# Optimization experiments

Measured on AMD Instinct MI355X. Metric: run time of the kernel, lower is better.

## Reference

```python
import jax, jax.numpy as jnp
import numpy as np

SCALING = 32.0 / 16.0  # alpha / rank


def _nf4_levels():
    # q_i = Phi^{-1}((i+0.5)/16), normalized to [-1, 1]
    i = jnp.arange(16, dtype=jnp.float32)
    p = jnp.clip((i + 0.5) / 16.0, 1e-6, 1.0 - 1e-6)
    lv = jnp.sqrt(2.0) * jax.scipy.special.erfinv(2.0 * p - 1.0)
    return lv / jnp.max(jnp.abs(lv))


def _dequantize(q_weight, scales):
    # q_weight: (out, in//2) packed nibbles; scales: (out, num_groups)
    out_f, packed = q_weight.shape
    in_f = packed * 2
    hi = (q_weight >> 4) & 15
    lo = q_weight & 15
    idx = jnp.stack([hi, lo], axis=-1).reshape(out_f, in_f)  # interleave hi/lo
    w = _nf4_levels()[idx]  # (out, in)
    num_groups = scales.shape[1]
    block = in_f // num_groups
    w = (w.reshape(out_f, num_groups, block) * scales[:, :, None].astype(jnp.float32))
    return w.reshape(out_f, in_f)


def setup_inputs() -> dict:
    key = jax.random.key(0)
    k1, k2, k3, k4, k5 = jax.random.split(key, 5)
    B, S, IN, OUT, R, BLK = 4, 64, 8192, 8192, 16, 64
    x = jax.random.normal(k1, (B, S, IN), dtype=jnp.float32)
    q_weight = jax.random.randint(k2, (OUT, IN // 2), 0, 256, dtype=jnp.int32)
    scales = jax.random.uniform(k3, (OUT, IN // BLK), dtype=jnp.float32) * 0.02 + 1e-4
    lora_A = jax.random.normal(k4, (R, IN), dtype=jnp.float32) * 0.02
    lora_B = jax.random.normal(k5, (OUT, R), dtype=jnp.float32) * 0.02
    return {"x": x, "q_weight": q_weight, "scales": scales,
            "lora_A": lora_A, "lora_B": lora_B}


def reference(x, q_weight, scales, lora_A, lora_B):
    w = _dequantize(q_weight, scales)               # (out, in) fp32
    base = jnp.einsum('bsi,oi->bso', x, w)          # F.linear(x, W)
    lora = jnp.einsum('bsi,ri->bsr', x, lora_A)     # x @ A^T (dropout p=0)
    lora = jnp.einsum('bsr,or->bso', lora, lora_B)  # @ B^T
    return base + SCALING * lora
```

## Files before the change

### kernel.cpp

```cpp
#include <hip/hip_runtime.h>
#include <hip/hip_bf16.h>
#include <stdint.h>

typedef __attribute__((ext_vector_type(4))) float f32x4;
typedef __attribute__((ext_vector_type(8))) short short8;
typedef __attribute__((ext_vector_type(4))) int int4v;

#define IN_F   8192
#define OUT_F  8192
#define MROWS  256
#define BN     64
#define BK     64
#define NGRP   128
#define KTILES 32

__device__ unsigned short g_xb[MROWS * IN_F];
__device__ float          g_t[MROWS * 16];
__device__ float          g_part[4 * MROWS * OUT_F];

__device__ __constant__ float NF4_LVL[16] = {
  -1.0f,        -0.70756721f, -0.54221982f, -0.41681853f,
  -0.31090474f, -0.21594601f, -0.12734085f, -0.04209530f,
   0.04209530f,  0.12734085f,  0.21594601f,  0.31090474f,
   0.41681853f,  0.54221982f,  0.70756721f,  1.0f };

static __device__ inline uint32_t pkbf(float a, float b) {
  __bf16 ha = (__bf16)a, hb = (__bf16)b;
  return (uint32_t)__builtin_bit_cast(unsigned short, ha)
       | ((uint32_t)__builtin_bit_cast(unsigned short, hb) << 16);
}

__global__ __launch_bounds__(256) void k_convert(const float* __restrict__ x) {
  int d = blockIdx.x * 256 + threadIdx.x;
  int l15 = d & 15, sub = (d >> 4) & 3, kk = (d >> 6) & 1;
  int m16 = (d >> 7) & 15, kt = d >> 11;
  int r = m16 * 16 + l15;
  int k = kt * 64 + (kk * 4 + sub) * 8;
  const float* src = x + (size_t)r * IN_F + k;
  f32x4 v0 = *(const f32x4*)src;
  f32x4 v1 = *(const f32x4*)(src + 4);
  int4v ov;
  ov[0] = (int)pkbf(v0.x, v0.y); ov[1] = (int)pkbf(v0.z, v0.w);
  ov[2] = (int)pkbf(v1.x, v1.y); ov[3] = (int)pkbf(v1.z, v1.w);
  *(int4v*)(g_xb + (size_t)d * 8) = ov;
}

__global__ __launch_bounds__(256) void k_xa(const float* __restrict__ x,
                                            const float* __restrict__ lora_A) {
  int m = blockIdx.x, tid = threadIdx.x;
  float acc[16];
#pragma unroll
  for (int r = 0; r < 16; ++r) acc[r] = 0.f;
  const float* xr = x + (size_t)m * IN_F;
  for (int it = 0; it < 8; ++it) {
    int k = (tid + it * 256) * 4;
    f32x4 xv = *(const f32x4*)(xr + k);
#pragma unroll
    for (int r = 0; r < 16; ++r) {
      f32x4 av = *(const f32x4*)(lora_A + (size_t)r * IN_F + k);
      acc[r] += xv.x * av.x + xv.y * av.y + xv.z * av.z + xv.w * av.w;
    }
  }
#pragma unroll
  for (int r = 0; r < 16; ++r) {
    float v = acc[r];
#pragma unroll
    for (int off = 32; off; off >>= 1) v += __shfl_xor(v, off, 64);
    acc[r] = v;
  }
  __shared__ float sm[4][16];
  int lane = tid & 63, wave = tid >> 6;
  if (lane == 0) {
#pragma unroll
    for (int r = 0; r < 16; ++r) sm[wave][r] = acc[r];
  }
  __syncthreads();
  if (tid < 16)
    g_t[m * 16 + tid] = 2.0f * (sm[0][tid] + sm[1][tid] + sm[2][tid] + sm[3][tid]);
}

__global__ __launch_bounds__(512, 4) void k_gemm(
    const int* __restrict__ qw, const float* __restrict__ scales)
{
  __shared__ unsigned short Bl[2][BN * BK];
  __shared__ float lut16[16];

  int tid = threadIdx.x;
  int lane = tid & 63, wave = tid >> 6;
  if (tid < 16) lut16[tid] = NF4_LVL[tid];

  int flat = blockIdx.x;
  int wg = (flat & 7) * 64 + (flat >> 3);
  int bx = wg & 127, bz = wg >> 7;
  int n0 = bx * BN;
  int ktg0 = bz * KTILES;

  int dn = tid >> 3, dc = tid & 7;
  const int* qr = qw + (size_t)(n0 + dn) * (IN_F / 2) + dc * 4;
  const float* sr = scales + (size_t)(n0 + dn) * NGRP;
  int boff = dn * 128 + ((dc ^ (dn & 7)) << 4);

  f32x4 acc[4][2];
#pragma unroll
  for (int i = 0; i < 4; ++i)
#pragma unroll
    for (int j = 0; j < 2; ++j) acc[i][j] = (f32x4){0.f, 0.f, 0.f, 0.f};

  int wr = wave >> 1, wc = wave & 1;
  int wn = wc * 32;
  int sub = lane >> 4, l15 = lane & 15;
  int aoff = (wr * 4) * 1024 + (sub * 16 + l15) * 8;

  auto dqst = [&](int buf, int4v q, float s) {
    int4v ov;
#pragma unroll
    for (int e = 0; e < 4; ++e) {
      float hi = lut16[(q[e] >> 4) & 15];
      float lo = lut16[q[e] & 15];
      ov[e] = (int)pkbf(hi * s, lo * s);
    }
    *(int4v*)((char*)(&Bl[buf][0]) + boff) = ov;
  };

  __syncthreads();

  int4v qcur = *(const int4v*)(qr + ktg0 * 32);
  float scur = sr[ktg0];
  dqst(0, qcur, scur);
  int4v qnxt = *(const int4v*)(qr + (ktg0 + 1) * 32);
  float snxt = sr[ktg0 + 1];
  asm volatile("s_waitcnt lgkmcnt(0)" ::: "memory");
  __builtin_amdgcn_s_barrier();

#pragma clang loop unroll(disable)
  for (int t = 0; t < KTILES; ++t) {
    int cur = t & 1;
    int ktg = ktg0 + t;

    short8 bfv[2][2];
#pragma unroll
    for (int kk = 0; kk < 2; ++kk)
#pragma unroll
      for (int ni = 0; ni < 2; ++ni) {
        int n = wn + ni * 16 + l15;
        int cch = (kk * 4 + sub) ^ (n & 7);
        bfv[kk][ni] = *(const short8*)((const char*)(&Bl[cur][0]) + n * 128 + cch * 16);
      }

    short8 af[2][4];
    const unsigned short* ab = g_xb + (size_t)ktg * 16384;
#pragma unroll
    for (int kk = 0; kk < 2; ++kk)
#pragma unroll
      for (int mi = 0; mi < 4; ++mi)
        af[kk][mi] = *(const short8*)(ab + aoff + mi * 1024 + kk * 512);

    if (t < KTILES - 1) {
      int kn = ktg0 + ((t < KTILES - 2) ? (t + 2) : (KTILES - 1));
      int4v qn2 = *(const int4v*)(qr + kn * 32);
      float sn2 = sr[kn];
      dqst(cur ^ 1, qnxt, snxt);
      qnxt = qn2; snxt = sn2;
    }

    __builtin_amdgcn_s_setprio(1);
#pragma unroll
    for (int kk = 0; kk < 2; ++kk)
#pragma unroll
      for (int mi = 0; mi < 4; ++mi)
#pragma unroll
        for (int ni = 0; ni < 2; ++ni)
          acc[mi][ni] = __builtin_amdgcn_mfma_f32_16x16x32_bf16(
              af[kk][mi], bfv[kk][ni], acc[mi][ni], 0, 0, 0);
    __builtin_amdgcn_s_setprio(0);

    if (t < KTILES - 1) {
      asm volatile("s_waitcnt lgkmcnt(0)" ::: "memory");
      __builtin_amdgcn_s_barrier();
    }
  }

  float* op = g_part + (size_t)bz * MROWS * OUT_F;
#pragma unroll
  for (int mi = 0; mi < 4; ++mi) {
#pragma unroll
    for (int ni = 0; ni < 2; ++ni) {
      int m = wr * 64 + mi * 16 + sub * 4;
      int nn = n0 + wn + ni * 16 + l15;
#pragma unroll
      for (int j = 0; j < 4; ++j)
        op[(size_t)(m + j) * OUT_F + nn] = acc[mi][ni][j];
    }
  }
}

__global__ __launch_bounds__(256) void k_reduce(const float* __restrict__ lora_B,
                                                float* __restrict__ out) {
  size_t i = ((size_t)blockIdx.x * 256 + threadIdx.x) * 4;
  int m = (int)(i >> 13);
  int n = (int)(i & 8191);
  f32x4 v = *(const f32x4*)(g_part + i);
  v += *(const f32x4*)(g_part + (size_t)1 * MROWS * OUT_F + i);
  v += *(const f32x4*)(g_part + (size_t)2 * MROWS * OUT_F + i);
  v += *(const f32x4*)(g_part + (size_t)3 * MROWS * OUT_F + i);
  const float* tr = g_t + m * 16;
  f32x4 t0 = *(const f32x4*)tr,       t1 = *(const f32x4*)(tr + 4);
  f32x4 t2 = *(const f32x4*)(tr + 8), t3 = *(const f32x4*)(tr + 12);
#pragma unroll
  for (int j = 0; j < 4; ++j) {
    const float* br = lora_B + (size_t)(n + j) * 16;
    f32x4 b0 = *(const f32x4*)br,       b1 = *(const f32x4*)(br + 4);
    f32x4 b2 = *(const f32x4*)(br + 8), b3 = *(const f32x4*)(br + 12);
    v[j] += t0.x*b0.x + t0.y*b0.y + t0.z*b0.z + t0.w*b0.w
          + t1.x*b1.x + t1.y*b1.y + t1.z*b1.z + t1.w*b1.w
          + t2.x*b2.x + t2.y*b2.y + t2.z*b2.z + t2.w*b2.w
          + t3.x*b3.x + t3.y*b3.y + t3.z*b3.z + t3.w*b3.w;
  }
  *(f32x4*)(out + i) = v;
}

extern "C" void kernel_launch(void* const* d_in, const int* in_sizes, int n_in,
                              void* d_out, int out_size, void* d_ws, size_t ws_size,
                              hipStream_t stream) {
  const float* x  = (const float*)d_in[0];
  const int*   qw = (const int*)d_in[1];
  const float* sc = (const float*)d_in[2];
  const float* lA = (const float*)d_in[3];
  const float* lB = (const float*)d_in[4];
  float* out = (float*)d_out;

  k_convert<<<1024, 256, 0, stream>>>(x);
  k_xa<<<256, 256, 0, stream>>>(x, lA);
  k_gemm<<<512, 512, 0, stream>>>(qw, sc);
  k_reduce<<<2048, 256, 0, stream>>>(lB, out);
}
```

Before: 105.3 us.

## Dequantize NF4 weights directly into registers, drop LDS staging and barriers

The GEMM no longer stages dequantized weight tiles through shared memory. Each wave loads packed nibbles for its own 64 output columns, dequantizes them in registers with a 256-entry byte-pair LUT, and prefetches one K tile ahead. The block tile widens to 128 columns with half as many blocks, and per-tile barriers are removed. The cost is dequant work duplicated across the four row-waves, plus higher register pressure and lower occupancy.

```diff
diff --git a/kernel.cpp b/kernel.cpp
--- a/kernel.cpp
+++ b/kernel.cpp
@@ -9,9 +9,8 @@
 #define IN_F   8192
 #define OUT_F  8192
 #define MROWS  256
-#define BN     64
-#define BK     64
 #define NGRP   128
+#define QROW   4096
 #define KTILES 32
 
 __device__ unsigned short g_xb[MROWS * IN_F];
@@ -79,112 +78,111 @@
     g_t[m * 16 + tid] = 2.0f * (sm[0][tid] + sm[1][tid] + sm[2][tid] + sm[3][tid]);
 }
 
-__global__ __launch_bounds__(512, 4) void k_gemm(
+__global__ __launch_bounds__(512, 2) void k_gemm(
     const int* __restrict__ qw, const float* __restrict__ scales)
 {
-  __shared__ unsigned short Bl[2][BN * BK];
-  __shared__ float lut16[16];
-
+  __shared__ uint32_t lut2[256];
   int tid = threadIdx.x;
   int lane = tid & 63, wave = tid >> 6;
-  if (tid < 16) lut16[tid] = NF4_LVL[tid];
+  if (tid < 256) lut2[tid] = pkbf(NF4_LVL[tid >> 4], NF4_LVL[tid & 15]);
+  __syncthreads();
 
   int flat = blockIdx.x;
-  int wg = (flat & 7) * 64 + (flat >> 3);
-  int bx = wg & 127, bz = wg >> 7;
-  int n0 = bx * BN;
+  int wg = (flat & 7) * 32 + (flat >> 3);
+  int bx = wg & 63, bz = wg >> 6;
+  int n0 = bx * 128;
   int ktg0 = bz * KTILES;
 
-  int dn = tid >> 3, dc = tid & 7;
-  const int* qr = qw + (size_t)(n0 + dn) * (IN_F / 2) + dc * 4;
-  const float* sr = scales + (size_t)(n0 + dn) * NGRP;
-  int boff = dn * 128 + ((dc ^ (dn & 7)) << 4);
-
-  f32x4 acc[4][2];
+  int wr = wave >> 1;
+  int wc = wave & 1;
+  int wn = wc * 64;
+  int sub = lane >> 4, l15 = lane & 15;
+
+  size_t rowb = (size_t)(n0 + wn + l15);
+  const int* qbase = qw + rowb * QROW + sub * 4;
+  const float* sbase = scales + rowb * NGRP;
+
+  const unsigned short* abase =
+      g_xb + (size_t)ktg0 * 16384 + (wr * 4) * 1024 + (sub * 16 + l15) * 8;
+
+  f32x4 acc[4][4];
 #pragma unroll
   for (int i = 0; i < 4; ++i)
 #pragma unroll
-    for (int j = 0; j < 2; ++j) acc[i][j] = (f32x4){0.f, 0.f, 0.f, 0.f};
-
-  int wr = wave >> 1, wc = wave & 1;
-  int wn = wc * 32;
-  int sub = lane >> 4, l15 = lane & 15;
-  int aoff = (wr * 4) * 1024 + (sub * 16 + l15) * 8;
-
-  auto dqst = [&](int buf, int4v q, float s) {
-    int4v ov;
-#pragma unroll
-    for (int e = 0; e < 4; ++e) {
-      float hi = lut16[(q[e] >> 4) & 15];
-      float lo = lut16[q[e] & 15];
-      ov[e] = (int)pkbf(hi * s, lo * s);
-    }
-    *(int4v*)((char*)(&Bl[buf][0]) + boff) = ov;
-  };
-
-  __syncthreads();
-
-  int4v qcur = *(const int4v*)(qr + ktg0 * 32);
-  float scur = sr[ktg0];
-  dqst(0, qcur, scur);
-  int4v qnxt = *(const int4v*)(qr + (ktg0 + 1) * 32);
-  float snxt = sr[ktg0 + 1];
-  asm volatile("s_waitcnt lgkmcnt(0)" ::: "memory");
-  __builtin_amdgcn_s_barrier();
+    for (int j = 0; j < 4; ++j) acc[i][j] = (f32x4){0.f, 0.f, 0.f, 0.f};
+
+  int4v qb[8];
+  float sb[4];
+#pragma unroll
+  for (int ni = 0; ni < 4; ++ni) {
+    const int* qp = qbase + (size_t)ni * 16 * QROW + (size_t)ktg0 * 32;
+    qb[ni * 2 + 0] = *(const int4v*)qp;
+    qb[ni * 2 + 1] = *(const int4v*)(qp + 16);
+    sb[ni] = sbase[(size_t)ni * 16 * NGRP + ktg0];
+  }
 
 #pragma clang loop unroll(disable)
   for (int t = 0; t < KTILES; ++t) {
-    int cur = t & 1;
-    int ktg = ktg0 + t;
-
-    short8 bfv[2][2];
+    short8 af[2][4];
+    const unsigned short* ab = abase + (size_t)t * 16384;
 #pragma unroll
     for (int kk = 0; kk < 2; ++kk)
 #pragma unroll
-      for (int ni = 0; ni < 2; ++ni) {
-        int n = wn + ni * 16 + l15;
-        int cch = (kk * 4 + sub) ^ (n & 7);
-        bfv[kk][ni] = *(const short8*)((const char*)(&Bl[cur][0]) + n * 128 + cch * 16);
+      for (int mi = 0; mi < 4; ++mi)
+        af[kk][mi] = *(const short8*)(ab + mi * 1024 + kk * 512);
+
+    int tn = (t < KTILES - 1) ? (t + 1) : t;
+    size_t koff = (size_t)(ktg0 + tn) * 32;
+    int4v qn[8];
+    float sn[4];
+#pragma unroll
+    for (int ni = 0; ni < 4; ++ni) {
+      const int* qp = qbase + (size_t)ni * 16 * QROW + koff;
+      qn[ni * 2 + 0] = *(const int4v*)qp;
+      qn[ni * 2 + 1] = *(const int4v*)(qp + 16);
+      sn[ni] = sbase[(size_t)ni * 16 * NGRP + (ktg0 + tn)];
+    }
+
+    short8 bq[8];
+#pragma unroll
+    for (int ni = 0; ni < 4; ++ni) {
+      float s = sb[ni];
+#pragma unroll
+      for (int kk = 0; kk < 2; ++kk) {
+        int4v q = qb[ni * 2 + kk];
+        int4v ov;
+#pragma unroll
+        for (int e = 0; e < 4; ++e) {
+          uint32_t pk = lut2[q[e] & 255];
+          float fh = __builtin_bit_cast(float, pk << 16);
+          float fl = __builtin_bit_cast(float, pk & 0xFFFF0000u);
+          ov[e] = (int)pkbf(fh * s, fl * s);
+        }
+        bq[ni * 2 + kk] = __builtin_bit_cast(short8, ov);
       }
-
-    short8 af[2][4];
-    const unsigned short* ab = g_xb + (size_t)ktg * 16384;
+    }
+#pragma unroll
+    for (int i = 0; i < 8; ++i) qb[i] = qn[i];
+#pragma unroll
+    for (int i = 0; i < 4; ++i) sb[i] = sn[i];
+
+    __builtin_amdgcn_s_setprio(1);
 #pragma unroll
     for (int kk = 0; kk < 2; ++kk)
 #pragma unroll
       for (int mi = 0; mi < 4; ++mi)
-        af[kk][mi] = *(const short8*)(ab + aoff + mi * 1024 + kk * 512);
-
-    if (t < KTILES - 1) {
-      int kn = ktg0 + ((t < KTILES - 2) ? (t + 2) : (KTILES - 1));
-      int4v qn2 = *(const int4v*)(qr + kn * 32);
-      float sn2 = sr[kn];
-      dqst(cur ^ 1, qnxt, snxt);
-      qnxt = qn2; snxt = sn2;
-    }
-
-    __builtin_amdgcn_s_setprio(1);
-#pragma unroll
-    for (int kk = 0; kk < 2; ++kk)
-#pragma unroll
-      for (int mi = 0; mi < 4; ++mi)
-#pragma unroll
-        for (int ni = 0; ni < 2; ++ni)
+#pragma unroll
+        for (int ni = 0; ni < 4; ++ni)
           acc[mi][ni] = __builtin_amdgcn_mfma_f32_16x16x32_bf16(
-              af[kk][mi], bfv[kk][ni], acc[mi][ni], 0, 0, 0);
+              af[kk][mi], bq[ni * 2 + kk], acc[mi][ni], 0, 0, 0);
     __builtin_amdgcn_s_setprio(0);
-
-    if (t < KTILES - 1) {
-      asm volatile("s_waitcnt lgkmcnt(0)" ::: "memory");
-      __builtin_amdgcn_s_barrier();
-    }
   }
 
   float* op = g_part + (size_t)bz * MROWS * OUT_F;
 #pragma unroll
   for (int mi = 0; mi < 4; ++mi) {
 #pragma unroll
-    for (int ni = 0; ni < 2; ++ni) {
+    for (int ni = 0; ni < 4; ++ni) {
       int m = wr * 64 + mi * 16 + sub * 4;
       int nn = n0 + wn + ni * 16 + l15;
 #pragma unroll
@@ -231,6 +229,6 @@
 
   k_convert<<<1024, 256, 0, stream>>>(x);
   k_xa<<<256, 256, 0, stream>>>(x, lA);
-  k_gemm<<<512, 512, 0, stream>>>(qw, sc);
+  k_gemm<<<256, 512, 0, stream>>>(qw, sc);
   k_reduce<<<2048, 256, 0, stream>>>(lB, out);
 }
```

Measured after the change: 161.0 us. 53.0% more time.
